# Kernel optimization log

Measured on AMD Instinct MI355X. Metric: run time of the kernel, lower is better.

The kernel has to match this reference:

```python
import jax, jax.numpy as jnp
import numpy as np

N_FEATURES = 60
WINDOW = 64
N_FFT_BINS = WINDOW // 2 + 1  # 33
HIDDEN = 256
N_OUT = 3
TOTAL_IN = N_FEATURES + N_FEATURES * N_FFT_BINS  # 2040


def setup_inputs() -> dict:
    key = jax.random.key(0)
    ks = jax.random.split(key, 9)
    B, T = 4, 4096
    x = jax.random.normal(ks[0], (B, T, N_FEATURES), dtype=jnp.float32)

    def lin(k, fan_in, fan_out):
        bound = 1.0 / np.sqrt(fan_in)
        kw, kb = jax.random.split(k)
        W = jax.random.uniform(kw, (fan_in, fan_out), minval=-bound, maxval=bound, dtype=jnp.float32)
        b = jax.random.uniform(kb, (fan_out,), minval=-bound, maxval=bound, dtype=jnp.float32)
        return W, b

    W1, b1 = lin(ks[1], TOTAL_IN, HIDDEN)
    W2, b2 = lin(ks[2], HIDDEN, HIDDEN)
    W3, b3 = lin(ks[3], HIDDEN, HIDDEN // 2)
    W4, b4 = lin(ks[4], HIDDEN // 2, N_OUT)
    return {"x": x, "W1": W1, "b1": b1, "W2": W2, "b2": b2,
            "W3": W3, "b3": b3, "W4": W4, "b4": b4}


def _fft_features(x):
    # x: [B, T, F]
    B, T, F = x.shape
    half_w = WINDOW // 2
    # reflect pad along time: (half_w, half_w - 1)
    xp = jnp.pad(x, ((0, 0), (half_w, half_w - 1), (0, 0)), mode='reflect')  # [B, T+W-1, F]
    # sliding windows: [B, T, W, F] -> [B, T, F, W] (matches torch unfold layout)
    idx = jnp.arange(T)[:, None] + jnp.arange(WINDOW)[None, :]  # [T, W]
    windows = xp[:, idx, :].transpose(0, 1, 3, 2)  # [B, T, F, W]
    fft_mag = jnp.log1p(jnp.abs(jnp.fft.rfft(windows, axis=-1)))  # [B, T, F, W//2+1]
    return fft_mag.reshape(B, T, F * N_FFT_BINS)


def reference(x, W1, b1, W2, b2, W3, b3, W4, b4):
    fft_flat = _fft_features(x)
    h = jnp.concatenate([x, fft_flat], axis=-1)  # [B, T, 2040]
    h = jax.nn.relu(h @ W1 + b1)   # dropout is identity in eval mode
    h = jax.nn.relu(h @ W2 + b2)
    h = jax.nn.relu(h @ W3 + b3)
    return h @ W4 + b4             # [B, T, 3]
```

## Files before the change

### kernel.cpp

```cpp
#include <hip/hip_runtime.h>
#include <math.h>

#define T_LEN 4096
#define NF 60
#define NBINS 33
#define KPAD 2048
#define HID 256
#define NTOK 16384
#define LINE 4208

typedef _Float16 half_t;
typedef half_t half8 __attribute__((ext_vector_type(8)));
typedef half_t half4 __attribute__((ext_vector_type(4)));
typedef float f32x4 __attribute__((ext_vector_type(4)));

constexpr double K_PI = 3.14159265358979323846;
constexpr double tcos(double x) {
    while (x >  K_PI) x -= 2.0 * K_PI;
    while (x < -K_PI) x += 2.0 * K_PI;
    double x2 = x * x, s = 0.0, term = 1.0;
    for (int m = 0; m < 14; ++m) { s += term; term *= -x2 / ((2.0*m + 1.0) * (2.0*m + 2.0)); }
    return s;
}
struct CosTab { float v[64]; };
constexpr CosTab make_tab() {
    CosTab t{};
    for (int j = 0; j < 64; ++j) t.v[j] = (float)tcos(2.0 * K_PI * (double)j / 64.0);
    return t;
}
__device__ constexpr CosTab CTd = make_tab();

__device__ __forceinline__ float log2_1p(float x) {
    return __log2f(1.0f + x);
}

__global__ __launch_bounds__(256) void prep_kernel(
        const float* __restrict__ W1, const float* __restrict__ W2,
        const float* __restrict__ W3,
        half_t* __restrict__ dftH,
        half_t* __restrict__ W1T, half_t* __restrict__ W2T,
        half_t* __restrict__ W3T) {
    int i = blockIdx.x * 256 + threadIdx.x;
    if (i < 4096) {
        int row = i >> 6, n = i & 63;
        float c = (row < 33) ? CTd.v[(row * n) & 63]
                             : CTd.v[((row - 32) * n + 48) & 63];
        dftH[i] = (half_t)c;
        return;
    }
    i -= 4096;
    if (i < 256 * KPAD) {
        int gk = i & (KPAD - 1);
        float v = 0.f;
        if (gk < 2040) {
            int j = i >> 11;
            int r;
            bool isfft = true;
            if (gk < 1920) {
                int f = gk >> 5, bin = gk & 31;
                r = NF + f * NBINS + bin;
            } else if (gk < 1980) {
                r = gk - 1920; isfft = false;
            } else {
                r = NF + (gk - 1980) * NBINS + 32;
            }
            v = W1[(size_t)r * HID + j];
            if (isfft) v *= 0.69314718055994531f;
        }
        W1T[i] = (half_t)v;
        return;
    }
    i -= 256 * KPAD;
    if (i < 256 * 256) {
        int k = i & 255, j = i >> 8;
        W2T[i] = (half_t)W2[(size_t)k * HID + j];
        return;
    }
    i -= 256 * 256;
    if (i < 128 * 256) {
        int k = i & 255, j = i >> 8;
        W3T[i] = (half_t)W3[(size_t)k * 128 + j];
    }
}

__global__ __launch_bounds__(256) void xline_kernel(
        const float* __restrict__ x, half_t* __restrict__ lineG) {
    const int bf = blockIdx.x;
    const int b = bf / NF, f = bf - b * NF;
    const float* xb = x + (size_t)b * T_LEN * NF + f;
    half_t* L = lineG + (size_t)bf * LINE;
    for (int j = threadIdx.x; j < LINE; j += 256) {
        int s = j - 32;
        int r = (s < 0) ? -s : ((s > T_LEN - 1) ? 2 * (T_LEN - 1) - s : s);
        L[j] = (half_t)xb[(size_t)r * NF];
    }
}

__global__ __launch_bounds__(256) void raw_kernel(
        const float* __restrict__ x, half_t* __restrict__ H0) {
    const int t = blockIdx.x * 256 + threadIdx.x;
    const int b = t >> 12, tl = t & (T_LEN - 1);
    const int i = (b << 12) + ((tl & 7) << 9) + (tl >> 3);
    const float* xp = x + (size_t)t * NF;
    half_t* hp = H0 + (size_t)i * KPAD;
#pragma unroll
    for (int f4 = 0; f4 < 15; ++f4) {
        float4 v = *(const float4*)(xp + f4 * 4);
        half4 h;
        h[0] = (half_t)v.x; h[1] = (half_t)v.y;
        h[2] = (half_t)v.z; h[3] = (half_t)v.w;
        *(half4*)&hp[1920 + f4 * 4] = h;
    }
    half8 z = {};
    *(half8*)&hp[2040] = z;
}

__global__ __launch_bounds__(256) void fft_hankel(
        const half_t* __restrict__ lineG, const half_t* __restrict__ dftH,
        half_t* __restrict__ H0) {
    __shared__ half_t L[2176];

    const int bid = blockIdx.x;
    const int bf = bid >> 4, c = (bid >> 1) & 7, hf = bid & 1;
    const int b = bf / NF, f = bf - b * NF;
    const int tid = threadIdx.x;
    const int lane = tid & 63, wv = tid >> 6;
    const int lr = lane & 15, lg = lane >> 4;

    half8 a[4][2];
#pragma unroll
    for (int rf = 0; rf < 4; ++rf)
#pragma unroll
        for (int ks = 0; ks < 2; ++ks)
            a[rf][ks] = *(const half8*)&dftH[(16 * rf + lr) * 64 + ks * 32 + lg * 8];

    {
        const half_t* src = lineG + (size_t)bf * LINE + hf * 2048 + c;
        for (int j = tid; j < 2144; j += 256) L[j] = src[j];
    }
    __syncthreads();

    const int i0 = (b << 12) + (c << 9) + (hf << 8);

#pragma unroll
    for (int cs = 0; cs < 4; ++cs) {
        const int s0 = wv * 64 + cs * 16;
        half8 w0 = *(const half8*)&L[8 * (s0 + lr) + lg * 8];
        half8 w1 = *(const half8*)&L[8 * (s0 + lr) + 32 + lg * 8];
        f32x4 dacc[4] = {};
#pragma unroll
        for (int rf = 0; rf < 4; ++rf)
            dacc[rf] = __builtin_amdgcn_mfma_f32_16x16x32_f16(a[rf][0], w0, dacc[rf], 0, 0, 0);
#pragma unroll
        for (int rf = 0; rf < 4; ++rf)
            dacc[rf] = __builtin_amdgcn_mfma_f32_16x16x32_f16(a[rf][1], w1, dacc[rf], 0, 0, 0);

        half_t* base = H0 + (size_t)(i0 + s0 + lr) * KPAD;
#pragma unroll
        for (int rf = 0; rf < 2; ++rf) {
            half4 h4;
#pragma unroll
            for (int r = 0; r < 4; ++r) {
                float re = dacc[rf][r];
                float im = dacc[rf + 2][r];
                float v = (rf == 0 && r == 0)
                    ? ((lg == 0) ? log2_1p(fabsf(re))
                                 : log2_1p(sqrtf(re * re + im * im)))
                    : log2_1p(sqrtf(re * re + im * im));
                h4[r] = (half_t)v;
            }
            *(half4*)&base[f * 32 + 16 * rf + 4 * lg] = h4;
        }
        if (lg == 0)
            base[1980 + f] = (half_t)log2_1p(fabsf(dacc[2][0]));
    }
}

template<int BN, bool OUT_F32>
__global__ __launch_bounds__(256, 2) void gemm_pipe(
        const half_t* __restrict__ A, int lda,
        const half_t* __restrict__ BT, int ldb,
        const float* __restrict__ bias,
        half_t* __restrict__ Ch, float* __restrict__ Cf,
        int N, int K) {
    constexpr int NFR = BN / 64;
    __shared__ half_t As[2][64 * 64];

    const int tid  = threadIdx.x;
    const int row0 = blockIdx.x * 64;
    const int col0 = blockIdx.y * BN;
    const int wv = tid >> 6, lane = tid & 63;
    const int lr = lane & 15, lg = lane >> 4;

    const int srow = tid >> 2, sg = (tid & 3) * 2;
    const int wo0 = srow * 64 + ((sg ^ (srow & 7)) * 8);
    const int wo1 = srow * 64 + (((sg + 1) ^ (srow & 7)) * 8);
    const half_t* ap = A + (size_t)(row0 + srow) * lda + sg * 8;

    const half_t* bp[NFR];
#pragma unroll
    for (int nf = 0; nf < NFR; ++nf)
        bp[nf] = BT + (size_t)(col0 + wv * (16 * NFR) + nf * 16 + lr) * ldb + lg * 8;

    f32x4 acc[4][NFR] = {};
    const int NIT = K / 64;

    half8 bcur[2][NFR], bnxt[2][NFR];
    half8 pa0, pa1, pb0, pb1;

    {
        half8 v0 = *(const half8*)(ap);
        half8 v1 = *(const half8*)(ap + 8);
        *(half8*)&As[0][wo0] = v0;
        *(half8*)&As[0][wo1] = v1;
    }
    if (NIT > 1) { pa0 = *(const half8*)(ap + 64);  pa1 = *(const half8*)(ap + 72); }
    if (NIT > 2) { pb0 = *(const half8*)(ap + 128); pb1 = *(const half8*)(ap + 136); }
#pragma unroll
    for (int ks = 0; ks < 2; ++ks)
#pragma unroll
        for (int nf = 0; nf < NFR; ++nf)
            bcur[ks][nf] = *(const half8*)(bp[nf] + ks * 32);

    for (int it = 0; it < NIT; it += 2) {
        __syncthreads();
        if (it + 1 < NIT) {
#pragma unroll
            for (int ks = 0; ks < 2; ++ks)
#pragma unroll
                for (int nf = 0; nf < NFR; ++nf)
                    bnxt[ks][nf] = *(const half8*)(bp[nf] + (it + 1) * 64 + ks * 32);
        }
#pragma unroll
        for (int ks = 0; ks < 2; ++ks) {
            half8 af[4];
#pragma unroll
            for (int mf = 0; mf < 4; ++mf)
                af[mf] = *(const half8*)&As[0][(mf * 16 + lr) * 64 + (((ks * 4 + lg) ^ (lr & 7)) * 8)];
#pragma unroll
            for (int mf = 0; mf < 4; ++mf)
#pragma unroll
                for (int nf = 0; nf < NFR; ++nf)
                    acc[mf][nf] = __builtin_amdgcn_mfma_f32_16x16x32_f16(af[mf], bcur[ks][nf], acc[mf][nf], 0, 0, 0);
        }
        if (it + 1 < NIT) { *(half8*)&As[1][wo0] = pa0; *(half8*)&As[1][wo1] = pa1; }
        if (it + 3 < NIT) { pa0 = *(const half8*)(ap + (it + 3) * 64); pa1 = *(const half8*)(ap + (it + 3) * 64 + 8); }
        if (it + 1 >= NIT) break;

        __syncthreads();
        if (it + 2 < NIT) {
#pragma unroll
            for (int ks = 0; ks < 2; ++ks)
#pragma unroll
                for (int nf = 0; nf < NFR; ++nf)
                    bcur[ks][nf] = *(const half8*)(bp[nf] + (it + 2) * 64 + ks * 32);
        }
#pragma unroll
        for (int ks = 0; ks < 2; ++ks) {
            half8 af[4];
#pragma unroll
            for (int mf = 0; mf < 4; ++mf)
                af[mf] = *(const half8*)&As[1][(mf * 16 + lr) * 64 + (((ks * 4 + lg) ^ (lr & 7)) * 8)];
#pragma unroll
            for (int mf = 0; mf < 4; ++mf)
#pragma unroll
                for (int nf = 0; nf < NFR; ++nf)
                    acc[mf][nf] = __builtin_amdgcn_mfma_f32_16x16x32_f16(af[mf], bnxt[ks][nf], acc[mf][nf], 0, 0, 0);
        }
        if (it + 2 < NIT) { *(half8*)&As[0][wo0] = pb0; *(half8*)&As[0][wo1] = pb1; }
        if (it + 4 < NIT) { pb0 = *(const half8*)(ap + (it + 4) * 64); pb1 = *(const half8*)(ap + (it + 4) * 64 + 8); }
    }

#pragma unroll
    for (int nf = 0; nf < NFR; ++nf) {
        int col = col0 + wv * (16 * NFR) + nf * 16 + lr;
        float bs = bias[col];
#pragma unroll
        for (int mf = 0; mf < 4; ++mf)
#pragma unroll
            for (int r = 0; r < 4; ++r) {
                int row = row0 + mf * 16 + lg * 4 + r;
                float v = fmaxf(acc[mf][nf][r] + bs, 0.f);
                if (OUT_F32) Cf[(size_t)row * N + col] = v;
                else         Ch[(size_t)row * N + col] = (half_t)v;
            }
    }
}

__global__ __launch_bounds__(256) void head_kernel(
        const float* __restrict__ H, const float* __restrict__ W4,
        const float* __restrict__ b4, float* __restrict__ out) {
    __shared__ float Ws[128 * 3];
    __shared__ float bs[3];
    for (int i = threadIdx.x; i < 384; i += 256) Ws[i] = W4[i];
    if (threadIdx.x < 3) bs[threadIdx.x] = b4[threadIdx.x];
    __syncthreads();
    const int i = blockIdx.x * 256 + threadIdx.x;
    const float* h = H + (size_t)i * 128;
    float a0 = bs[0], a1 = bs[1], a2 = bs[2];
#pragma unroll
    for (int k = 0; k < 128; ++k) {
        float hv = h[k];
        a0 = fmaf(hv, Ws[k * 3 + 0], a0);
        a1 = fmaf(hv, Ws[k * 3 + 1], a1);
        a2 = fmaf(hv, Ws[k * 3 + 2], a2);
    }
    const int b = i >> 12, c = (i >> 9) & 7, s = i & 511;
    const int t = (b << 12) + (s << 3) + c;
    float* o = out + (size_t)t * 3;
    o[0] = a0; o[1] = a1; o[2] = a2;
}

extern "C" void kernel_launch(void* const* d_in, const int* in_sizes, int n_in,
                              void* d_out, int out_size, void* d_ws, size_t ws_size,
                              hipStream_t stream) {
    (void)in_sizes; (void)n_in; (void)out_size; (void)ws_size;
    const float* x  = (const float*)d_in[0];
    const float* W1 = (const float*)d_in[1];
    const float* b1 = (const float*)d_in[2];
    const float* W2 = (const float*)d_in[3];
    const float* b2 = (const float*)d_in[4];
    const float* W3 = (const float*)d_in[5];
    const float* b3 = (const float*)d_in[6];
    const float* W4 = (const float*)d_in[7];
    const float* b4 = (const float*)d_in[8];
    float* out = (float*)d_out;

    char* w = (char*)d_ws;
    half_t* H0    = (half_t*)(w);
    half_t* H1    = (half_t*)(w + (size_t)64 * 1024 * 1024);
    half_t* H2    = (half_t*)(w + (size_t)72 * 1024 * 1024);
    float*  H3    = (float*) (w + (size_t)80 * 1024 * 1024);
    half_t* W1T   = (half_t*)(w + (size_t)88 * 1024 * 1024);
    half_t* W2T   = (half_t*)(w + (size_t)89 * 1024 * 1024);
    half_t* W3T   = W2T + 256 * 256;
    half_t* dftH  = W3T + 128 * 256;
    half_t* lineG = (half_t*)(w + (size_t)90 * 1024 * 1024);

    prep_kernel<<<2448, 256, 0, stream>>>(W1, W2, W3, dftH, W1T, W2T, W3T);
    xline_kernel<<<240, 256, 0, stream>>>(x, lineG);
    raw_kernel<<<NTOK / 256, 256, 0, stream>>>(x, H0);
    fft_hankel<<<240 * 16, 256, 0, stream>>>(lineG, dftH, H0);

    gemm_pipe<128, false><<<dim3(NTOK / 64, 2), 256, 0, stream>>>(
        H0, KPAD, W1T, KPAD, b1, H1, nullptr, HID, KPAD);
    gemm_pipe<128, false><<<dim3(NTOK / 64, 2), 256, 0, stream>>>(
        H1, HID, W2T, HID, b2, H2, nullptr, HID, HID);
    gemm_pipe<64, true><<<dim3(NTOK / 64, 2), 256, 0, stream>>>(
        H2, HID, W3T, HID, b3, nullptr, H3, HID / 2, HID);

    head_kernel<<<NTOK / 256, 256, 0, stream>>>(H3, W4, b4, out);
}
```

Measured before the change: 117.3 us.

## Fuse layer-3 GEMM with output head, merge prep kernels, enlarge FFT blocks

Merges the padded-line and raw-feature conversion kernels into one launch. It also halves the fft_hankel grid so each block handles a full 512-step chunk, prefetching the next window fragment while storing the current one. The third GEMM is fused with the 128-to-3 output head: the ReLU'd tile is staged in shared memory and reduced with shuffles, so the fp32 H3 buffer round trip and one kernel launch go away. The cost is more shared memory per block and a single-column-block grid for the fused layer.

```diff
diff --git a/kernel.cpp b/kernel.cpp
--- a/kernel.cpp
+++ b/kernel.cpp
@@ -83,22 +83,22 @@
     }
 }
 
-__global__ __launch_bounds__(256) void xline_kernel(
-        const float* __restrict__ x, half_t* __restrict__ lineG) {
-    const int bf = blockIdx.x;
-    const int b = bf / NF, f = bf - b * NF;
-    const float* xb = x + (size_t)b * T_LEN * NF + f;
-    half_t* L = lineG + (size_t)bf * LINE;
-    for (int j = threadIdx.x; j < LINE; j += 256) {
-        int s = j - 32;
-        int r = (s < 0) ? -s : ((s > T_LEN - 1) ? 2 * (T_LEN - 1) - s : s);
-        L[j] = (half_t)xb[(size_t)r * NF];
-    }
-}
-
-__global__ __launch_bounds__(256) void raw_kernel(
-        const float* __restrict__ x, half_t* __restrict__ H0) {
-    const int t = blockIdx.x * 256 + threadIdx.x;
+__global__ __launch_bounds__(256) void xr_kernel(
+        const float* __restrict__ x, half_t* __restrict__ lineG,
+        half_t* __restrict__ H0) {
+    if (blockIdx.x < 240) {
+        const int bf = blockIdx.x;
+        const int b = bf / NF, f = bf - b * NF;
+        const float* xb = x + (size_t)b * T_LEN * NF + f;
+        half_t* L = lineG + (size_t)bf * LINE;
+        for (int j = threadIdx.x; j < LINE; j += 256) {
+            int s = j - 32;
+            int r = (s < 0) ? -s : ((s > T_LEN - 1) ? 2 * (T_LEN - 1) - s : s);
+            L[j] = (half_t)xb[(size_t)r * NF];
+        }
+        return;
+    }
+    const int t = (blockIdx.x - 240) * 256 + threadIdx.x;
     const int b = t >> 12, tl = t & (T_LEN - 1);
     const int i = (b << 12) + ((tl & 7) << 9) + (tl >> 3);
     const float* xp = x + (size_t)t * NF;
@@ -118,10 +118,10 @@
 __global__ __launch_bounds__(256) void fft_hankel(
         const half_t* __restrict__ lineG, const half_t* __restrict__ dftH,
         half_t* __restrict__ H0) {
-    __shared__ half_t L[2176];
+    __shared__ half_t L[4160];
 
     const int bid = blockIdx.x;
-    const int bf = bid >> 4, c = (bid >> 1) & 7, hf = bid & 1;
+    const int bf = bid >> 3, c = bid & 7;
     const int b = bf / NF, f = bf - b * NF;
     const int tid = threadIdx.x;
     const int lane = tid & 63, wv = tid >> 6;
@@ -135,18 +135,19 @@
             a[rf][ks] = *(const half8*)&dftH[(16 * rf + lr) * 64 + ks * 32 + lg * 8];
 
     {
-        const half_t* src = lineG + (size_t)bf * LINE + hf * 2048 + c;
-        for (int j = tid; j < 2144; j += 256) L[j] = src[j];
+        const half_t* src = lineG + (size_t)bf * LINE + c;
+        for (int j = tid; j < 4152; j += 256) L[j] = src[j];
     }
     __syncthreads();
 
-    const int i0 = (b << 12) + (c << 9) + (hf << 8);
-
-#pragma unroll
-    for (int cs = 0; cs < 4; ++cs) {
-        const int s0 = wv * 64 + cs * 16;
-        half8 w0 = *(const half8*)&L[8 * (s0 + lr) + lg * 8];
-        half8 w1 = *(const half8*)&L[8 * (s0 + lr) + 32 + lg * 8];
+    const int i0 = (b << 12) + (c << 9);
+    const int sl = wv * 128 + lr;
+
+    half8 w0 = *(const half8*)&L[8 * sl + lg * 8];
+    half8 w1 = *(const half8*)&L[8 * sl + 32 + lg * 8];
+
+#pragma unroll
+    for (int cs = 0; cs < 8; ++cs) {
         f32x4 dacc[4] = {};
 #pragma unroll
         for (int rf = 0; rf < 4; ++rf)
@@ -155,7 +156,13 @@
         for (int rf = 0; rf < 4; ++rf)
             dacc[rf] = __builtin_amdgcn_mfma_f32_16x16x32_f16(a[rf][1], w1, dacc[rf], 0, 0, 0);
 
-        half_t* base = H0 + (size_t)(i0 + s0 + lr) * KPAD;
+        if (cs < 7) {
+            const int sn = sl + (cs + 1) * 16;
+            w0 = *(const half8*)&L[8 * sn + lg * 8];
+            w1 = *(const half8*)&L[8 * sn + 32 + lg * 8];
+        }
+
+        half_t* base = H0 + (size_t)(i0 + sl + cs * 16) * KPAD;
 #pragma unroll
         for (int rf = 0; rf < 2; ++rf) {
             half4 h4;
@@ -176,13 +183,12 @@
     }
 }
 
-template<int BN, bool OUT_F32>
+template<int BN>
 __global__ __launch_bounds__(256, 2) void gemm_pipe(
         const half_t* __restrict__ A, int lda,
         const half_t* __restrict__ BT, int ldb,
         const float* __restrict__ bias,
-        half_t* __restrict__ Ch, float* __restrict__ Cf,
-        int N, int K) {
+        half_t* __restrict__ Ch, int N, int K) {
     constexpr int NFR = BN / 64;
     __shared__ half_t As[2][64 * 64];
 
@@ -280,35 +286,135 @@
 #pragma unroll
             for (int r = 0; r < 4; ++r) {
                 int row = row0 + mf * 16 + lg * 4 + r;
-                float v = fmaxf(acc[mf][nf][r] + bs, 0.f);
-                if (OUT_F32) Cf[(size_t)row * N + col] = v;
-                else         Ch[(size_t)row * N + col] = (half_t)v;
+                Ch[(size_t)row * N + col] = (half_t)fmaxf(acc[mf][nf][r] + bs, 0.f);
             }
     }
 }
 
-__global__ __launch_bounds__(256) void head_kernel(
-        const float* __restrict__ H, const float* __restrict__ W4,
+__global__ __launch_bounds__(256) void gemm3_head(
+        const half_t* __restrict__ A, const half_t* __restrict__ BT,
+        const float* __restrict__ b3, const float* __restrict__ W4,
         const float* __restrict__ b4, float* __restrict__ out) {
-    __shared__ float Ws[128 * 3];
-    __shared__ float bs[3];
-    for (int i = threadIdx.x; i < 384; i += 256) Ws[i] = W4[i];
-    if (threadIdx.x < 3) bs[threadIdx.x] = b4[threadIdx.x];
+    constexpr int NFR = 2, NIT = 4;
+    __shared__ half_t As[2][64 * 64];
+    __shared__ float Hs[64][132];
+    __shared__ float W4s[384];
+
+    const int tid  = threadIdx.x;
+    const int row0 = blockIdx.x * 64;
+    const int wv = tid >> 6, lane = tid & 63;
+    const int lr = lane & 15, lg = lane >> 4;
+
+    for (int i = tid; i < 384; i += 256) W4s[i] = W4[i];
+
+    const int srow = tid >> 2, sg = (tid & 3) * 2;
+    const int wo0 = srow * 64 + ((sg ^ (srow & 7)) * 8);
+    const int wo1 = srow * 64 + (((sg + 1) ^ (srow & 7)) * 8);
+    const half_t* ap = A + (size_t)(row0 + srow) * 256 + sg * 8;
+
+    const half_t* bp[NFR];
+#pragma unroll
+    for (int nf = 0; nf < NFR; ++nf)
+        bp[nf] = BT + (size_t)(wv * 32 + nf * 16 + lr) * 256 + lg * 8;
+
+    f32x4 acc[4][NFR] = {};
+    half8 bcur[2][NFR], bnxt[2][NFR];
+    half8 pa0, pa1, pb0, pb1;
+
+    {
+        half8 v0 = *(const half8*)(ap);
+        half8 v1 = *(const half8*)(ap + 8);
+        *(half8*)&As[0][wo0] = v0;
+        *(half8*)&As[0][wo1] = v1;
+    }
+    pa0 = *(const half8*)(ap + 64);  pa1 = *(const half8*)(ap + 72);
+    pb0 = *(const half8*)(ap + 128); pb1 = *(const half8*)(ap + 136);
+#pragma unroll
+    for (int ks = 0; ks < 2; ++ks)
+#pragma unroll
+        for (int nf = 0; nf < NFR; ++nf)
+            bcur[ks][nf] = *(const half8*)(bp[nf] + ks * 32);
+
+    for (int it = 0; it < NIT; it += 2) {
+        __syncthreads();
+        if (it + 1 < NIT) {
+#pragma unroll
+            for (int ks = 0; ks < 2; ++ks)
+#pragma unroll
+                for (int nf = 0; nf < NFR; ++nf)
+                    bnxt[ks][nf] = *(const half8*)(bp[nf] + (it + 1) * 64 + ks * 32);
+        }
+#pragma unroll
+        for (int ks = 0; ks < 2; ++ks) {
+            half8 af[4];
+#pragma unroll
+            for (int mf = 0; mf < 4; ++mf)
+                af[mf] = *(const half8*)&As[0][(mf * 16 + lr) * 64 + (((ks * 4 + lg) ^ (lr & 7)) * 8)];
+#pragma unroll
+            for (int mf = 0; mf < 4; ++mf)
+#pragma unroll
+                for (int nf = 0; nf < NFR; ++nf)
+                    acc[mf][nf] = __builtin_amdgcn_mfma_f32_16x16x32_f16(af[mf], bcur[ks][nf], acc[mf][nf], 0, 0, 0);
+        }
+        if (it + 1 < NIT) { *(half8*)&As[1][wo0] = pa0; *(half8*)&As[1][wo1] = pa1; }
+        if (it + 3 < NIT) { pa0 = *(const half8*)(ap + (it + 3) * 64); pa1 = *(const half8*)(ap + (it + 3) * 64 + 8); }
+        if (it + 1 >= NIT) break;
+
+        __syncthreads();
+        if (it + 2 < NIT) {
+#pragma unroll
+            for (int ks = 0; ks < 2; ++ks)
+#pragma unroll
+                for (int nf = 0; nf < NFR; ++nf)
+                    bcur[ks][nf] = *(const half8*)(bp[nf] + (it + 2) * 64 + ks * 32);
+        }
+#pragma unroll
+        for (int ks = 0; ks < 2; ++ks) {
+            half8 af[4];
+#pragma unroll
+            for (int mf = 0; mf < 4; ++mf)
+                af[mf] = *(const half8*)&As[1][(mf * 16 + lr) * 64 + (((ks * 4 + lg) ^ (lr & 7)) * 8)];
+#pragma unroll
+            for (int mf = 0; mf < 4; ++mf)
+#pragma unroll
+                for (int nf = 0; nf < NFR; ++nf)
+                    acc[mf][nf] = __builtin_amdgcn_mfma_f32_16x16x32_f16(af[mf], bnxt[ks][nf], acc[mf][nf], 0, 0, 0);
+        }
+        if (it + 2 < NIT) { *(half8*)&As[0][wo0] = pb0; *(half8*)&As[0][wo1] = pb1; }
+        if (it + 4 < NIT) { pb0 = *(const half8*)(ap + (it + 4) * 64); pb1 = *(const half8*)(ap + (it + 4) * 64 + 8); }
+    }
+
+#pragma unroll
+    for (int nf = 0; nf < NFR; ++nf) {
+        int col = wv * 32 + nf * 16 + lr;
+        float bs = b3[col];
+#pragma unroll
+        for (int mf = 0; mf < 4; ++mf)
+#pragma unroll
+            for (int r = 0; r < 4; ++r)
+                Hs[mf * 16 + lg * 4 + r][col] = fmaxf(acc[mf][nf][r] + bs, 0.f);
+    }
     __syncthreads();
-    const int i = blockIdx.x * 256 + threadIdx.x;
-    const float* h = H + (size_t)i * 128;
-    float a0 = bs[0], a1 = bs[1], a2 = bs[2];
-#pragma unroll
-    for (int k = 0; k < 128; ++k) {
-        float hv = h[k];
-        a0 = fmaf(hv, Ws[k * 3 + 0], a0);
-        a1 = fmaf(hv, Ws[k * 3 + 1], a1);
-        a2 = fmaf(hv, Ws[k * 3 + 2], a2);
-    }
-    const int b = i >> 12, c = (i >> 9) & 7, s = i & 511;
-    const int t = (b << 12) + (s << 3) + c;
-    float* o = out + (size_t)t * 3;
-    o[0] = a0; o[1] = a1; o[2] = a2;
+
+    const int row = tid >> 2, q = tid & 3;
+    float a0 = 0.f, a1 = 0.f, a2 = 0.f;
+#pragma unroll
+    for (int k = 0; k < 32; ++k) {
+        float hv = Hs[row][q * 32 + k];
+        a0 = fmaf(hv, W4s[(q * 32 + k) * 3 + 0], a0);
+        a1 = fmaf(hv, W4s[(q * 32 + k) * 3 + 1], a1);
+        a2 = fmaf(hv, W4s[(q * 32 + k) * 3 + 2], a2);
+    }
+    a0 += __shfl_xor(a0, 1); a0 += __shfl_xor(a0, 2);
+    a1 += __shfl_xor(a1, 1); a1 += __shfl_xor(a1, 2);
+    a2 += __shfl_xor(a2, 1); a2 += __shfl_xor(a2, 2);
+    if (q == 0) {
+        const int i = row0 + row;
+        const int b = i >> 12, c = (i >> 9) & 7, s = i & 511;
+        const int t = (b << 12) + (s << 3) + c;
+        float* o = out + (size_t)t * 3;
+        o[0] = a0 + b4[0]; o[1] = a1 + b4[1]; o[2] = a2 + b4[2];
+    }
 }
 
 extern "C" void kernel_launch(void* const* d_in, const int* in_sizes, int n_in,
@@ -330,7 +436,6 @@
     half_t* H0    = (half_t*)(w);
     half_t* H1    = (half_t*)(w + (size_t)64 * 1024 * 1024);
     half_t* H2    = (half_t*)(w + (size_t)72 * 1024 * 1024);
-    float*  H3    = (float*) (w + (size_t)80 * 1024 * 1024);
     half_t* W1T   = (half_t*)(w + (size_t)88 * 1024 * 1024);
     half_t* W2T   = (half_t*)(w + (size_t)89 * 1024 * 1024);
     half_t* W3T   = W2T + 256 * 256;
@@ -338,16 +443,12 @@
     half_t* lineG = (half_t*)(w + (size_t)90 * 1024 * 1024);
 
     prep_kernel<<<2448, 256, 0, stream>>>(W1, W2, W3, dftH, W1T, W2T, W3T);
-    xline_kernel<<<240, 256, 0, stream>>>(x, lineG);
-    raw_kernel<<<NTOK / 256, 256, 0, stream>>>(x, H0);
-    fft_hankel<<<240 * 16, 256, 0, stream>>>(lineG, dftH, H0);
-
-    gemm_pipe<128, false><<<dim3(NTOK / 64, 2), 256, 0, stream>>>(
-        H0, KPAD, W1T, KPAD, b1, H1, nullptr, HID, KPAD);
-    gemm_pipe<128, false><<<dim3(NTOK / 64, 2), 256, 0, stream>>>(
-        H1, HID, W2T, HID, b2, H2, nullptr, HID, HID);
-    gemm_pipe<64, true><<<dim3(NTOK / 64, 2), 256, 0, stream>>>(
-        H2, HID, W3T, HID, b3, nullptr, H3, HID / 2, HID);
-
-    head_kernel<<<NTOK / 256, 256, 0, stream>>>(H3, W4, b4, out);
-}
+    xr_kernel<<<304, 256, 0, stream>>>(x, lineG, H0);
+    fft_hankel<<<240 * 8, 256, 0, stream>>>(lineG, dftH, H0);
+
+    gemm_pipe<128><<<dim3(NTOK / 64, 2), 256, 0, stream>>>(
+        H0, KPAD, W1T, KPAD, b1, H1, HID, KPAD);
+    gemm_pipe<128><<<dim3(NTOK / 64, 2), 256, 0, stream>>>(
+        H1, HID, W2T, HID, b2, H2, HID, HID);
+    gemm3_head<<<NTOK / 64, 256, 0, stream>>>(H2, W3T, b3, W4, b4, out);
+}
```

Measured after the change: 102.7 us. 1.14x faster.
